# Performance work log

Measured on AMD Instinct MI355X. Metric: run time of the kernel, lower is better.

The kernel has to match this reference:

```python
import jax, jax.numpy as jnp
import numpy as np

CHANNELS = [4096, 4096, 4096, 4096]
SPARSITY = 0.9  # fraction of weight entries zeroed (sten.random_mask_sparsify frac)
BATCH = 4096


def _sparse_weight(key, out_f, in_f, frac):
    kw, km = jax.random.split(key)
    w = jax.random.normal(kw, (out_f, in_f), dtype=jnp.float32)
    keep = jax.random.uniform(km, (out_f, in_f)) >= frac  # keep ~(1-frac) entries
    return jnp.where(keep, w, 0.0)


def setup_inputs() -> dict:
    key = jax.random.key(0)
    ks = jax.random.split(key, 7)
    x = jax.random.normal(ks[0], (BATCH, CHANNELS[0]), dtype=jnp.float32)
    W1 = _sparse_weight(ks[1], CHANNELS[1], CHANNELS[0], SPARSITY)
    b1 = jax.random.uniform(ks[2], (CHANNELS[1],), dtype=jnp.float32)
    W2 = _sparse_weight(ks[3], CHANNELS[2], CHANNELS[1], SPARSITY)
    b2 = jax.random.uniform(ks[4], (CHANNELS[2],), dtype=jnp.float32)
    W3 = _sparse_weight(ks[5], CHANNELS[3], CHANNELS[2], SPARSITY)
    b3 = jax.random.uniform(ks[6], (CHANNELS[3],), dtype=jnp.float32)
    return {"x": x, "W1": W1, "b1": b1, "W2": W2, "b2": b2, "W3": W3, "b3": b3}


def reference(x, W1, b1, W2, b2, W3, b3):
    # Sequential: Linear -> ReLU -> Linear -> ReLU -> Linear
    # F.linear(x, W, b) == x @ W.T + b; weights already carry the sparsity mask.
    h = x @ W1.T + b1
    h = jax.nn.relu(h)
    h = h @ W2.T + b2
    h = jax.nn.relu(h)
    return h @ W3.T + b3
```

## Files before the change

kernel.cpp:

```cpp
#include <hip/hip_runtime.h>
#include <cstdint>


#define MATN 4096

typedef _Float16 half8 __attribute__((ext_vector_type(8)));
typedef float f32x4 __attribute__((ext_vector_type(4)));

__device__ __forceinline__ void glds16(const void* g, void* l) {
    __builtin_amdgcn_global_load_lds(
        (const __attribute__((address_space(1))) char*)(uintptr_t)g,
        (__attribute__((address_space(3))) char*)(uintptr_t)l,
        16, 0, 0);
}

__device__ __forceinline__ void cvt_body(const float* __restrict__ in,
                                         _Float16* __restrict__ out, int n8) {
    for (int g = blockIdx.x * 256 + threadIdx.x; g < n8; g += gridDim.x * 256) {
        size_t i = (size_t)g * 8;
        float4 a = *(const float4*)(in + i);
        float4 b = *(const float4*)(in + i + 4);
        half8 o;
        o[0] = (_Float16)a.x; o[1] = (_Float16)a.y;
        o[2] = (_Float16)a.z; o[3] = (_Float16)a.w;
        o[4] = (_Float16)b.x; o[5] = (_Float16)b.y;
        o[6] = (_Float16)b.z; o[7] = (_Float16)b.w;
        *(half8*)(out + i) = o;
    }
}

__global__ __launch_bounds__(256)
void cvt_f16(const float* __restrict__ in, _Float16* __restrict__ out, int n8) {
    cvt_body(in, out, n8);
}

__global__ __launch_bounds__(256)
void cvt_f16_2(const float* __restrict__ i0, _Float16* __restrict__ o0,
               const float* __restrict__ i1, _Float16* __restrict__ o1, int n8) {
    cvt_body(blockIdx.y ? i1 : i0, blockIdx.y ? o1 : o0, n8);
}

template <bool RELU, typename OutT>
__global__ __launch_bounds__(256, 4)
void gemm_bt(const _Float16* __restrict__ A, const _Float16* __restrict__ B,
             const float* __restrict__ bias, OutT* __restrict__ C) {
    __shared__ _Float16 sA[128 * 64];
    __shared__ _Float16 sB[128 * 64];

    const int tid  = threadIdx.x;
    const int lane = tid & 63;
    const int w    = tid >> 6;
    const int wm   = w >> 1;
    const int wn   = w & 1;
    const int l16  = lane & 15;
    const int kq   = lane >> 4;

    const int tileM = blockIdx.y * 128;
    const int tileN = blockIdx.x * 128;

    f32x4 acc[4][4] = {};

    const int rin = tid >> 3;
    const int gch = (tid & 7) ^ (rin & 7);
    const _Float16* Ap = A + (size_t)(tileM + rin) * MATN + gch * 8;
    const _Float16* Bp = B + (size_t)(tileN + rin) * MATN + gch * 8;
    const size_t rstep = (size_t)32 * MATN;

    char* sAl = (char*)sA + w * 1024;
    char* sBl = (char*)sB + w * 1024;

    const int sl0 = kq ^ (l16 & 7);
    const int sl1 = sl0 ^ 4;
    const _Float16* rA0 = sA + (wm * 64 + l16) * 64 + sl0 * 8;
    const _Float16* rA1 = sA + (wm * 64 + l16) * 64 + sl1 * 8;
    const _Float16* rB0 = sB + (wn * 64 + l16) * 64 + sl0 * 8;
    const _Float16* rB1 = sB + (wn * 64 + l16) * 64 + sl1 * 8;

    for (int k0 = 0; k0 < MATN; k0 += 64) {
#pragma unroll
        for (int c = 0; c < 4; ++c) glds16(Ap + c * rstep, sAl + c * 4096);
#pragma unroll
        for (int c = 0; c < 4; ++c) glds16(Bp + c * rstep, sBl + c * 4096);
        Ap += 64; Bp += 64;
        __syncthreads();

        half8 af[4], bf[4];
#pragma unroll
        for (int mi = 0; mi < 4; ++mi) af[mi] = *(const half8*)(rA0 + mi * 1024);
#pragma unroll
        for (int ni = 0; ni < 4; ++ni) bf[ni] = *(const half8*)(rB0 + ni * 1024);
#pragma unroll
        for (int mi = 0; mi < 4; ++mi)
#pragma unroll
            for (int ni = 0; ni < 4; ++ni)
                acc[mi][ni] = __builtin_amdgcn_mfma_f32_16x16x32_f16(
                    af[mi], bf[ni], acc[mi][ni], 0, 0, 0);
#pragma unroll
        for (int mi = 0; mi < 4; ++mi) af[mi] = *(const half8*)(rA1 + mi * 1024);
#pragma unroll
        for (int ni = 0; ni < 4; ++ni) bf[ni] = *(const half8*)(rB1 + ni * 1024);
#pragma unroll
        for (int mi = 0; mi < 4; ++mi)
#pragma unroll
            for (int ni = 0; ni < 4; ++ni)
                acc[mi][ni] = __builtin_amdgcn_mfma_f32_16x16x32_f16(
                    af[mi], bf[ni], acc[mi][ni], 0, 0, 0);
        __syncthreads();
    }

#pragma unroll
    for (int ni = 0; ni < 4; ++ni) {
        const int gn = tileN + wn * 64 + ni * 16 + l16;
        const float bv = bias[gn];
#pragma unroll
        for (int mi = 0; mi < 4; ++mi) {
            const int gm = tileM + wm * 64 + mi * 16 + kq * 4;
#pragma unroll
            for (int r = 0; r < 4; ++r) {
                float v = acc[mi][ni][r] + bv;
                if (RELU) v = v > 0.f ? v : 0.f;
                C[(size_t)(gm + r) * MATN + gn] = (OutT)v;
            }
        }
    }
}

extern "C" void kernel_launch(void* const* d_in, const int* in_sizes, int n_in,
                              void* d_out, int out_size, void* d_ws, size_t ws_size,
                              hipStream_t stream) {
    const float* x  = (const float*)d_in[0];
    const float* W1 = (const float*)d_in[1];
    const float* b1 = (const float*)d_in[2];
    const float* W2 = (const float*)d_in[3];
    const float* b2 = (const float*)d_in[4];
    const float* W3 = (const float*)d_in[5];
    const float* b3 = (const float*)d_in[6];
    float* out = (float*)d_out;

    const size_t MAT = (size_t)MATN * MATN;
    _Float16* xb = (_Float16*)d_ws;
    _Float16* wb = (_Float16*)((char*)d_ws + MAT * 2);
    _Float16* h1 = (_Float16*)((char*)d_ws + MAT * 4);
    _Float16* h2 = xb;

    const int n8 = (int)(MAT / 8);
    dim3 ggrid(MATN / 128, MATN / 128);

    cvt_f16_2<<<dim3(2048, 2), 256, 0, stream>>>(x, xb, W1, wb, n8);
    gemm_bt<true, _Float16><<<ggrid, 256, 0, stream>>>(xb, wb, b1, h1);

    cvt_f16<<<2048, 256, 0, stream>>>(W2, wb, n8);
    gemm_bt<true, _Float16><<<ggrid, 256, 0, stream>>>(h1, wb, b2, h2);

    cvt_f16<<<2048, 256, 0, stream>>>(W3, wb, n8);
    gemm_bt<false, float><<<ggrid, 256, 0, stream>>>(h2, wb, b3, out);
}
```

Baseline: 594.3 us.

## Rewrite GEMM as 256x256 tile, 8-wave, double-buffered pipeline with batched conversions

The GEMM kernel moves from a 128x128 tile with 4 waves to a 256x256 tile with 8 waves. The tile's K loop is split into four quarter-stages that are double-buffered in LDS, with global-to-LDS loads issued ahead of compute, explicit waitcnt and barriers, and s_setprio around MFMA bursts. Blocks are remapped with an XCD-aware swizzle. When workspace allows, all four fp32->fp16 conversions run in a single launch. The aim is to hide load latency and raise MFMA utilisation, at the cost of more LDS, more registers and lower occupancy.

Result: faster. 571.8 us (-3.8%).

```diff
diff --git a/kernel.cpp b/kernel.cpp
--- a/kernel.cpp
+++ b/kernel.cpp
@@ -3,6 +3,7 @@
 
 
 #define MATN 4096
+#define NT (MATN / 64)
 
 typedef _Float16 half8 __attribute__((ext_vector_type(8)));
 typedef float f32x4 __attribute__((ext_vector_type(4)));
@@ -40,81 +41,177 @@
     cvt_body(blockIdx.y ? i1 : i0, blockIdx.y ? o1 : o0, n8);
 }
 
+__global__ __launch_bounds__(256)
+void cvt_f16_4(const float* __restrict__ i0, _Float16* __restrict__ o0,
+               const float* __restrict__ i1, _Float16* __restrict__ o1,
+               const float* __restrict__ i2, _Float16* __restrict__ o2,
+               const float* __restrict__ i3, _Float16* __restrict__ o3, int n8) {
+    const float* in;
+    _Float16* out;
+    switch (blockIdx.y) {
+        case 0: in = i0; out = o0; break;
+        case 1: in = i1; out = o1; break;
+        case 2: in = i2; out = o2; break;
+        default: in = i3; out = o3; break;
+    }
+    cvt_body(in, out, n8);
+}
+
+#define MFMA_(d, x, y) d = __builtin_amdgcn_mfma_f32_16x16x32_f16(x, y, d, 0, 0, 0)
+
 template <bool RELU, typename OutT>
-__global__ __launch_bounds__(256, 4)
+__global__ __launch_bounds__(512, 2)
 void gemm_bt(const _Float16* __restrict__ A, const _Float16* __restrict__ B,
              const float* __restrict__ bias, OutT* __restrict__ C) {
-    __shared__ _Float16 sA[128 * 64];
-    __shared__ _Float16 sB[128 * 64];
+    __shared__ _Float16 lds[2][4][128 * 64];
 
     const int tid  = threadIdx.x;
     const int lane = tid & 63;
     const int w    = tid >> 6;
-    const int wm   = w >> 1;
-    const int wn   = w & 1;
+    const int wm   = w >> 2;
+    const int wn   = w & 3;
     const int l16  = lane & 15;
     const int kq   = lane >> 4;
 
-    const int tileM = blockIdx.y * 128;
-    const int tileN = blockIdx.x * 128;
-
-    f32x4 acc[4][4] = {};
+    const int bid   = blockIdx.y * 16 + blockIdx.x;
+    const int sbid  = (bid & 7) * 32 + (bid >> 3);
+    const int tileM = (sbid >> 4) * 256;
+    const int tileN = (sbid & 15) * 256;
 
     const int rin = tid >> 3;
     const int gch = (tid & 7) ^ (rin & 7);
-    const _Float16* Ap = A + (size_t)(tileM + rin) * MATN + gch * 8;
-    const _Float16* Bp = B + (size_t)(tileN + rin) * MATN + gch * 8;
-    const size_t rstep = (size_t)32 * MATN;
-
-    char* sAl = (char*)sA + w * 1024;
-    char* sBl = (char*)sB + w * 1024;
-
-    const int sl0 = kq ^ (l16 & 7);
-    const int sl1 = sl0 ^ 4;
-    const _Float16* rA0 = sA + (wm * 64 + l16) * 64 + sl0 * 8;
-    const _Float16* rA1 = sA + (wm * 64 + l16) * 64 + sl1 * 8;
-    const _Float16* rB0 = sB + (wn * 64 + l16) * 64 + sl0 * 8;
-    const _Float16* rB1 = sB + (wn * 64 + l16) * 64 + sl1 * 8;
-
-    for (int k0 = 0; k0 < MATN; k0 += 64) {
-#pragma unroll
-        for (int c = 0; c < 4; ++c) glds16(Ap + c * rstep, sAl + c * 4096);
-#pragma unroll
-        for (int c = 0; c < 4; ++c) glds16(Bp + c * rstep, sBl + c * 4096);
-        Ap += 64; Bp += 64;
-        __syncthreads();
-
-        half8 af[4], bf[4];
-#pragma unroll
-        for (int mi = 0; mi < 4; ++mi) af[mi] = *(const half8*)(rA0 + mi * 1024);
-#pragma unroll
-        for (int ni = 0; ni < 4; ++ni) bf[ni] = *(const half8*)(rB0 + ni * 1024);
-#pragma unroll
-        for (int mi = 0; mi < 4; ++mi)
-#pragma unroll
-            for (int ni = 0; ni < 4; ++ni)
-                acc[mi][ni] = __builtin_amdgcn_mfma_f32_16x16x32_f16(
-                    af[mi], bf[ni], acc[mi][ni], 0, 0, 0);
-#pragma unroll
-        for (int mi = 0; mi < 4; ++mi) af[mi] = *(const half8*)(rA1 + mi * 1024);
-#pragma unroll
-        for (int ni = 0; ni < 4; ++ni) bf[ni] = *(const half8*)(rB1 + ni * 1024);
-#pragma unroll
-        for (int mi = 0; mi < 4; ++mi)
-#pragma unroll
-            for (int ni = 0; ni < 4; ++ni)
-                acc[mi][ni] = __builtin_amdgcn_mfma_f32_16x16x32_f16(
-                    af[mi], bf[ni], acc[mi][ni], 0, 0, 0);
-        __syncthreads();
-    }
+    char* const ldsb = (char*)lds;
+    const int wq = w * 1024;
+
+    const _Float16* const arow = A + (size_t)(tileM + rin) * MATN + gch * 8;
+    const _Float16* const brow = B + (size_t)(tileN + rin) * MATN + gch * 8;
+
+#define STAGE(Tt, s, rowp, roff)                                               \
+    do {                                                                       \
+        if ((Tt) < NT) {                                                       \
+            const _Float16* g_ = (rowp) + (size_t)(roff) * MATN + (Tt) * 64;   \
+            char* l_ = ldsb + ((((Tt) & 1) * 4 + (s)) * 16384) + wq;           \
+            glds16(g_, l_);                                                    \
+            glds16(g_ + (size_t)64 * MATN, l_ + 8192);                         \
+        }                                                                      \
+    } while (0)
+
+    const int rbA = (wm * 16 + l16) * 128;
+    const int rbB = (wn * 16 + l16) * 128;
+    const int ok0 = (kq ^ (l16 & 7)) * 16;
+    const int ok1 = ok0 ^ 64;
+
+    half8 a[4][2], b0[2][2], b1[2][2];
+    f32x4 acc[8][4] = {};
+
+    STAGE(0, 0, arow, 0);
+    STAGE(0, 1, brow, 0);
+    STAGE(0, 2, brow, 128);
+    STAGE(0, 3, arow, 128);
+    STAGE(1, 0, arow, 0);
+    STAGE(1, 1, brow, 0);
+    STAGE(1, 2, brow, 128);
+    asm volatile("s_waitcnt vmcnt(6)" ::: "memory");
+    __builtin_amdgcn_s_barrier();
+
+#pragma unroll 2
+    for (int T = 0; T < NT; ++T) {
+        const char* bufA0 = ldsb + ((T & 1) * 4 + 0) * 16384;
+        const char* bufB0 = ldsb + ((T & 1) * 4 + 1) * 16384;
+        const char* bufB1 = ldsb + ((T & 1) * 4 + 2) * 16384;
+        const char* bufA1 = ldsb + ((T & 1) * 4 + 3) * 16384;
+
+#pragma unroll
+        for (int mi = 0; mi < 4; ++mi) {
+            a[mi][0] = *(const half8*)(bufA0 + mi * 4096 + rbA + ok0);
+            a[mi][1] = *(const half8*)(bufA0 + mi * 4096 + rbA + ok1);
+        }
+#pragma unroll
+        for (int ni = 0; ni < 2; ++ni) {
+            b0[ni][0] = *(const half8*)(bufB0 + ni * 8192 + rbB + ok0);
+            b0[ni][1] = *(const half8*)(bufB0 + ni * 8192 + rbB + ok1);
+        }
+        STAGE(T + 1, 3, arow, 128);
+        __builtin_amdgcn_s_barrier();
+        asm volatile("s_waitcnt lgkmcnt(0)" ::: "memory");
+        __builtin_amdgcn_sched_barrier(0);
+        __builtin_amdgcn_s_setprio(1);
+#pragma unroll
+        for (int mi = 0; mi < 4; ++mi)
+#pragma unroll
+            for (int ni = 0; ni < 2; ++ni) {
+                MFMA_(acc[mi][ni], a[mi][0], b0[ni][0]);
+                MFMA_(acc[mi][ni], a[mi][1], b0[ni][1]);
+            }
+        __builtin_amdgcn_s_setprio(0);
+        __builtin_amdgcn_s_barrier();
+
+#pragma unroll
+        for (int ni = 0; ni < 2; ++ni) {
+            b1[ni][0] = *(const half8*)(bufB1 + ni * 8192 + rbB + ok0);
+            b1[ni][1] = *(const half8*)(bufB1 + ni * 8192 + rbB + ok1);
+        }
+        STAGE(T + 2, 0, arow, 0);
+        __builtin_amdgcn_s_barrier();
+        asm volatile("s_waitcnt lgkmcnt(0)" ::: "memory");
+        __builtin_amdgcn_sched_barrier(0);
+        __builtin_amdgcn_s_setprio(1);
+#pragma unroll
+        for (int mi = 0; mi < 4; ++mi)
+#pragma unroll
+            for (int ni = 0; ni < 2; ++ni) {
+                MFMA_(acc[mi][2 + ni], a[mi][0], b1[ni][0]);
+                MFMA_(acc[mi][2 + ni], a[mi][1], b1[ni][1]);
+            }
+        __builtin_amdgcn_s_setprio(0);
+        __builtin_amdgcn_s_barrier();
+
+#pragma unroll
+        for (int mi = 0; mi < 4; ++mi) {
+            a[mi][0] = *(const half8*)(bufA1 + mi * 4096 + rbA + ok0);
+            a[mi][1] = *(const half8*)(bufA1 + mi * 4096 + rbA + ok1);
+        }
+        STAGE(T + 2, 1, brow, 0);
+        __builtin_amdgcn_s_barrier();
+        asm volatile("s_waitcnt lgkmcnt(0)" ::: "memory");
+        __builtin_amdgcn_sched_barrier(0);
+        __builtin_amdgcn_s_setprio(1);
+#pragma unroll
+        for (int mi = 0; mi < 4; ++mi)
+#pragma unroll
+            for (int ni = 0; ni < 2; ++ni) {
+                MFMA_(acc[4 + mi][2 + ni], a[mi][0], b1[ni][0]);
+                MFMA_(acc[4 + mi][2 + ni], a[mi][1], b1[ni][1]);
+            }
+        __builtin_amdgcn_s_setprio(0);
+        __builtin_amdgcn_s_barrier();
+
+        STAGE(T + 2, 2, brow, 128);
+        __builtin_amdgcn_s_barrier();
+        __builtin_amdgcn_s_setprio(1);
+#pragma unroll
+        for (int mi = 0; mi < 4; ++mi)
+#pragma unroll
+            for (int ni = 0; ni < 2; ++ni) {
+                MFMA_(acc[4 + mi][ni], a[mi][0], b0[ni][0]);
+                MFMA_(acc[4 + mi][ni], a[mi][1], b0[ni][1]);
+            }
+        __builtin_amdgcn_s_setprio(0);
+        if (T < NT - 2)
+            asm volatile("s_waitcnt vmcnt(6)" ::: "memory");
+        else if (T == NT - 2)
+            asm volatile("s_waitcnt vmcnt(0)" ::: "memory");
+        __builtin_amdgcn_s_barrier();
+    }
+#undef STAGE
 
 #pragma unroll
     for (int ni = 0; ni < 4; ++ni) {
-        const int gn = tileN + wn * 64 + ni * 16 + l16;
+        const int gn = tileN + ni * 64 + wn * 16 + l16;
         const float bv = bias[gn];
 #pragma unroll
-        for (int mi = 0; mi < 4; ++mi) {
-            const int gm = tileM + wm * 64 + mi * 16 + kq * 4;
+        for (int mi = 0; mi < 8; ++mi) {
+            const int gm = tileM + mi * 32 + wm * 16 + kq * 4;
 #pragma unroll
             for (int r = 0; r < 4; ++r) {
                 float v = acc[mi][ni][r] + bv;
@@ -138,20 +235,34 @@
     float* out = (float*)d_out;
 
     const size_t MAT = (size_t)MATN * MATN;
-    _Float16* xb = (_Float16*)d_ws;
-    _Float16* wb = (_Float16*)((char*)d_ws + MAT * 2);
-    _Float16* h1 = (_Float16*)((char*)d_ws + MAT * 4);
-    _Float16* h2 = xb;
-
+    const size_t HB  = MAT * 2;
     const int n8 = (int)(MAT / 8);
-    dim3 ggrid(MATN / 128, MATN / 128);
-
-    cvt_f16_2<<<dim3(2048, 2), 256, 0, stream>>>(x, xb, W1, wb, n8);
-    gemm_bt<true, _Float16><<<ggrid, 256, 0, stream>>>(xb, wb, b1, h1);
-
-    cvt_f16<<<2048, 256, 0, stream>>>(W2, wb, n8);
-    gemm_bt<true, _Float16><<<ggrid, 256, 0, stream>>>(h1, wb, b2, h2);
-
-    cvt_f16<<<2048, 256, 0, stream>>>(W3, wb, n8);
-    gemm_bt<false, float><<<ggrid, 256, 0, stream>>>(h2, wb, b3, out);
-}
+    dim3 ggrid(MATN / 256, MATN / 256);
+
+    if (ws_size >= HB * 5) {
+        _Float16* xb = (_Float16*)d_ws;
+        _Float16* w1 = (_Float16*)((char*)d_ws + HB);
+        _Float16* w2 = (_Float16*)((char*)d_ws + HB * 2);
+        _Float16* w3 = (_Float16*)((char*)d_ws + HB * 3);
+        _Float16* h1 = (_Float16*)((char*)d_ws + HB * 4);
+        _Float16* h2 = xb;
+
+        cvt_f16_4<<<dim3(2048, 4), 256, 0, stream>>>(x, xb, W1, w1, W2, w2,
+                                                     W3, w3, n8);
+        gemm_bt<true, _Float16><<<ggrid, 512, 0, stream>>>(xb, w1, b1, h1);
+        gemm_bt<true, _Float16><<<ggrid, 512, 0, stream>>>(h1, w2, b2, h2);
+        gemm_bt<false, float><<<ggrid, 512, 0, stream>>>(h2, w3, b3, out);
+    } else {
+        _Float16* xb = (_Float16*)d_ws;
+        _Float16* wb = (_Float16*)((char*)d_ws + HB);
+        _Float16* h1 = (_Float16*)((char*)d_ws + HB * 2);
+        _Float16* h2 = xb;
+
+        cvt_f16_2<<<dim3(2048, 2), 256, 0, stream>>>(x, xb, W1, wb, n8);
+        gemm_bt<true, _Float16><<<ggrid, 512, 0, stream>>>(xb, wb, b1, h1);
+        cvt_f16<<<2048, 256, 0, stream>>>(W2, wb, n8);
+        gemm_bt<true, _Float16><<<ggrid, 512, 0, stream>>>(h1, wb, b2, h2);
+        cvt_f16<<<2048, 256, 0, stream>>>(W3, wb, n8);
+        gemm_bt<false, float><<<ggrid, 512, 0, stream>>>(h2, wb, b3, out);
+    }
+}
```
